# Kernel optimization log

Hardware: AMD Instinct MI355X
Metric: run time of the kernel (lower is better)

The kernel has to match this reference:

```python
import jax, jax.numpy as jnp
import numpy as np

N = 50000
E = 1_600_000
IN_C, HID_C, OUT_C = 128, 64, 16
NEG_SLOPE = 0.2


def setup_inputs() -> dict:
    key = jax.random.key(0)
    ks = jax.random.split(key, 16)
    x = jax.random.normal(ks[0], (N, IN_C), dtype=jnp.float32)
    edge_index = jax.random.randint(ks[1], (2, E), 0, N, dtype=jnp.int32)
    edge_weight = jax.random.uniform(ks[2], (E,), dtype=jnp.float32)

    def lin(k, fan_in, fan_out):
        s = (6.0 / (fan_in + fan_out)) ** 0.5
        return jax.random.uniform(k, (fan_in, fan_out), jnp.float32, -s, s)

    params = {
        "W1": lin(ks[3], IN_C, HID_C),
        "a_src1": jax.random.normal(ks[4], (HID_C,), jnp.float32) * 0.1,
        "a_dst1": jax.random.normal(ks[5], (HID_C,), jnp.float32) * 0.1,
        "b1": jnp.zeros((HID_C,), jnp.float32),
        "W2": lin(ks[6], HID_C, HID_C),
        "a_src2": jax.random.normal(ks[7], (HID_C,), jnp.float32) * 0.1,
        "a_dst2": jax.random.normal(ks[8], (HID_C,), jnp.float32) * 0.1,
        "b2": jnp.zeros((HID_C,), jnp.float32),
        "W3": lin(ks[9], HID_C, OUT_C),
        "a_src3": jax.random.normal(ks[10], (OUT_C,), jnp.float32) * 0.1,
        "a_dst3": jax.random.normal(ks[11], (OUT_C,), jnp.float32) * 0.1,
        "b3": jnp.zeros((OUT_C,), jnp.float32),
    }
    return {"x": x, "edge_index": edge_index, "edge_weight": edge_weight, **params}


def gat_conv(x, W, a_src, a_dst, b, src, dst):
    """Single-head PyG GATConv, add_self_loops=False, eval mode."""
    h = x @ W                                    # [N, C]
    alpha_src = (h * a_src).sum(-1)              # [N]
    alpha_dst = (h * a_dst).sum(-1)              # [N]
    e = jax.nn.leaky_relu(alpha_src[src] + alpha_dst[dst], NEG_SLOPE)  # [E]
    # softmax over incoming edges of each target node
    m = jax.ops.segment_max(e, dst, num_segments=N)
    e = jnp.exp(e - m[dst])
    denom = jax.ops.segment_sum(e, dst, num_segments=N)
    alpha = e / (denom[dst] + 1e-16)             # [E]
    out = jax.ops.segment_sum(h[src] * alpha[:, None], dst, num_segments=N)
    return out + b


def reference(x, edge_index, edge_weight,
              W1, a_src1, a_dst1, b1,
              W2, a_src2, a_dst2, b2,
              W3, a_src3, a_dst3, b3):
    src, dst = edge_index[0], edge_index[1]
    # edge_weight unused: GATConv has no lin_edge (edge_dim=None)
    h = jax.nn.relu(gat_conv(x, W1, a_src1, a_dst1, b1, src, dst))
    h = jax.nn.relu(gat_conv(h, W2, a_src2, a_dst2, b2, src, dst))
    return gat_conv(h, W3, a_src3, a_dst3, b3, src, dst)
```

## Files before the change

### kernel.cpp

```cpp
#include <hip/hip_runtime.h>
#include <hip/hip_fp16.h>
#include <math.h>

#define N_NODES 50000
#define N_EDGES 1600000
#define BSH 8
#define NBUCK ((N_NODES + 255) >> BSH)
#define EPB 4096
#define NBLK ((N_EDGES + EPB - 1) / EPB)


__global__ __launch_bounds__(256) void bucket_hist(const int* __restrict__ dst,
                                                   int* __restrict__ bhist_t, int e) {
    __shared__ int h[NBUCK];
    for (int i = threadIdx.x; i < NBUCK; i += 256) h[i] = 0;
    __syncthreads();
    int base = blockIdx.x * EPB;
#pragma unroll
    for (int j = 0; j < EPB / 256; ++j) {
        int i = base + j * 256 + threadIdx.x;
        if (i < e) atomicAdd(&h[dst[i] >> BSH], 1);
    }
    __syncthreads();
    for (int i = threadIdx.x; i < NBUCK; i += 256)
        bhist_t[i * NBLK + blockIdx.x] = h[i];
}

__global__ __launch_bounds__(256) void bucket_totals(const int* __restrict__ bhist_t,
                                                     int* __restrict__ btot) {
    int b = blockIdx.x;
    const int* col = bhist_t + (size_t)b * NBLK;
    int s = 0;
    for (int i = threadIdx.x; i < NBLK; i += 256) s += col[i];
#pragma unroll
    for (int off = 1; off < 64; off <<= 1) s += __shfl_xor(s, off);
    __shared__ int red[4];
    if ((threadIdx.x & 63) == 0) red[threadIdx.x >> 6] = s;
    __syncthreads();
    if (threadIdx.x == 0)
        btot[b] = red[0] + red[1] + red[2] + red[3];
}

__global__ __launch_bounds__(256) void scan_totals(const int* __restrict__ btot,
                                                   int* __restrict__ bbase,
                                                   int* __restrict__ rowptr) {
    __shared__ int s[256];
    int b = threadIdx.x;
    int v = (b < NBUCK) ? btot[b] : 0;
    s[b] = v;
    __syncthreads();
    for (int off = 1; off < 256; off <<= 1) {
        int t = (b >= off) ? s[b - off] : 0;
        __syncthreads();
        s[b] += t;
        __syncthreads();
    }
    if (b < NBUCK) bbase[b] = s[b] - v;
    if (b == NBUCK - 1) { bbase[NBUCK] = s[b]; rowptr[N_NODES] = s[b]; }
}

__global__ __launch_bounds__(64) void rewrite_offsets(int* __restrict__ bhist_t,
                                                      const int* __restrict__ bbase) {
    int b = blockIdx.x;
    int* col = bhist_t + (size_t)b * NBLK;
    __shared__ int buf[NBLK];
    for (int i = threadIdx.x; i < NBLK; i += 64) buf[i] = col[i];
    __syncthreads();
    constexpr int CH = (NBLK + 63) / 64;
    int lane = threadIdx.x;
    int lo = lane * CH;
    int hi = lo + CH; if (hi > NBLK) hi = NBLK;
    int s = 0;
    for (int i = lo; i < hi; ++i) s += buf[i];
    int inc = s;
#pragma unroll
    for (int off = 1; off < 64; off <<= 1) {
        int t = __shfl_up(inc, off);
        if (lane >= off) inc += t;
    }
    int run = bbase[b] + inc - s;
    for (int i = lo; i < hi; ++i) { int c = buf[i]; col[i] = run; run += c; }
}

__global__ __launch_bounds__(256) void bucket_scatter(const int* __restrict__ src,
                                                      const int* __restrict__ dst,
                                                      const int* __restrict__ bhist_t,
                                                      unsigned* __restrict__ packed, int e) {
    __shared__ int lcur[NBUCK];
    int r = blockIdx.x;
    for (int i = threadIdx.x; i < NBUCK; i += 256)
        lcur[i] = bhist_t[i * NBLK + r];
    __syncthreads();
    int base = r * EPB;
#pragma unroll
    for (int j = 0; j < EPB / 256; ++j) {
        int i = base + j * 256 + threadIdx.x;
        if (i < e) {
            int d = dst[i];
            int pos = atomicAdd(&lcur[d >> BSH], 1);
            packed[pos] = (unsigned)src[i] | ((unsigned)(d & ((1 << BSH) - 1)) << 16);
        }
    }
}

__global__ __launch_bounds__(512) void csr_finalize(const unsigned* __restrict__ packed,
                                                    const int* __restrict__ bbase,
                                                    int* __restrict__ rowptr,
                                                    int* __restrict__ csr_src) {
    int b = blockIdx.x;
    int s0 = bbase[b], s1 = bbase[b + 1];
    int cnt = s1 - s0;
    __shared__ int ncnt[256];
    __shared__ int ncur[256];
    __shared__ int wsum[4];
    if (threadIdx.x < 256) ncnt[threadIdx.x] = 0;
    __syncthreads();
    for (int i = threadIdx.x; i < cnt; i += 512)
        atomicAdd(&ncnt[packed[s0 + i] >> 16], 1);
    __syncthreads();
    int lane = threadIdx.x & 63, w = threadIdx.x >> 6;
    int v = 0, inc = 0;
    if (threadIdx.x < 256) {
        v = ncnt[threadIdx.x]; inc = v;
#pragma unroll
        for (int off = 1; off < 64; off <<= 1) {
            int t = __shfl_up(inc, off);
            if (lane >= off) inc += t;
        }
        if (lane == 63) wsum[w] = inc;
    }
    __syncthreads();
    if (threadIdx.x < 256) {
        int woff = 0;
#pragma unroll
        for (int k = 0; k < 3; ++k) if (k < w) woff += wsum[k];
        int excl = woff + inc - v;
        int node = (b << BSH) + threadIdx.x;
        if (node < N_NODES) rowptr[node] = s0 + excl;
        ncur[threadIdx.x] = s0 + excl;
    }
    __syncthreads();
    for (int i = threadIdx.x; i < cnt; i += 512) {
        unsigned p = packed[s0 + i];
        int pos = atomicAdd(&ncur[p >> 16], 1);
        csr_src[pos] = (int)(p & 0xFFFFu);
    }
}


template<int K, int C, bool HALF_OUT>
__global__ __launch_bounds__(256) void gemm_alpha(
        const float* __restrict__ in, const float* __restrict__ W,
        const float* __restrict__ a_src, const float* __restrict__ a_dst,
        void* __restrict__ hv, float* __restrict__ as_, float* __restrict__ ad_, int n)
{
    constexpr int CPT = C / 16;
    constexpr int KP = K + 4;
    __shared__ float sx[64][KP];
    __shared__ float sW[K * C];
    int row0 = blockIdx.x * 64;
    int nvalid = n - row0;

    for (int idx = threadIdx.x; idx < 64 * K / 4; idx += 256) {
        int r = idx / (K / 4), kc = idx % (K / 4);
        float4 v = {0, 0, 0, 0};
        if (r < nvalid) v = *(const float4*)&in[(size_t)(row0 + r) * K + kc * 4];
        *(float4*)&sx[r][kc * 4] = v;
    }
    for (int idx = threadIdx.x; idx < K * C / 4; idx += 256)
        *(float4*)&sW[idx * 4] = *(const float4*)&W[idx * 4];
    __syncthreads();

    int g  = threadIdx.x >> 4;
    int ci = threadIdx.x & 15;
    int r0 = g * 4;
    int c0 = ci * CPT;

    if constexpr (CPT == 4) {
        float4 acc0 = {0,0,0,0}, acc1 = {0,0,0,0}, acc2 = {0,0,0,0}, acc3 = {0,0,0,0};
        for (int k = 0; k < K; k += 4) {
            float4 w0 = *(const float4*)&sW[(k + 0) * C + c0];
            float4 w1 = *(const float4*)&sW[(k + 1) * C + c0];
            float4 w2 = *(const float4*)&sW[(k + 2) * C + c0];
            float4 w3 = *(const float4*)&sW[(k + 3) * C + c0];
            float4 x0 = *(const float4*)&sx[r0 + 0][k];
            float4 x1 = *(const float4*)&sx[r0 + 1][k];
            float4 x2 = *(const float4*)&sx[r0 + 2][k];
            float4 x3 = *(const float4*)&sx[r0 + 3][k];
#define STEP(A, X) \
            A.x = fmaf(X.x, w0.x, A.x); A.y = fmaf(X.x, w0.y, A.y); \
            A.z = fmaf(X.x, w0.z, A.z); A.w = fmaf(X.x, w0.w, A.w); \
            A.x = fmaf(X.y, w1.x, A.x); A.y = fmaf(X.y, w1.y, A.y); \
            A.z = fmaf(X.y, w1.z, A.z); A.w = fmaf(X.y, w1.w, A.w); \
            A.x = fmaf(X.z, w2.x, A.x); A.y = fmaf(X.z, w2.y, A.y); \
            A.z = fmaf(X.z, w2.z, A.z); A.w = fmaf(X.z, w2.w, A.w); \
            A.x = fmaf(X.w, w3.x, A.x); A.y = fmaf(X.w, w3.y, A.y); \
            A.z = fmaf(X.w, w3.z, A.z); A.w = fmaf(X.w, w3.w, A.w);
            STEP(acc0, x0) STEP(acc1, x1) STEP(acc2, x2) STEP(acc3, x3)
#undef STEP
        }
        if constexpr (HALF_OUT) {
            __half* hh = (__half*)hv;
            auto sth = [&](int r, float4 a) {
                if (r0 + r < nvalid) {
                    size_t base = (size_t)(row0 + r0 + r) * C + c0;
                    *(__half2*)&hh[base]     = __floats2half2_rn(a.x, a.y);
                    *(__half2*)&hh[base + 2] = __floats2half2_rn(a.z, a.w);
                }
            };
            sth(0, acc0); sth(1, acc1); sth(2, acc2); sth(3, acc3);
        } else {
            float* h = (float*)hv;
            if (r0 + 0 < nvalid) *(float4*)&h[(size_t)(row0 + r0 + 0) * C + c0] = acc0;
            if (r0 + 1 < nvalid) *(float4*)&h[(size_t)(row0 + r0 + 1) * C + c0] = acc1;
            if (r0 + 2 < nvalid) *(float4*)&h[(size_t)(row0 + r0 + 2) * C + c0] = acc2;
            if (r0 + 3 < nvalid) *(float4*)&h[(size_t)(row0 + r0 + 3) * C + c0] = acc3;
        }
        float4 asv = *(const float4*)&a_src[c0];
        float4 adv = *(const float4*)&a_dst[c0];
        float vs0 = acc0.x*asv.x + acc0.y*asv.y + acc0.z*asv.z + acc0.w*asv.w;
        float vs1 = acc1.x*asv.x + acc1.y*asv.y + acc1.z*asv.z + acc1.w*asv.w;
        float vs2 = acc2.x*asv.x + acc2.y*asv.y + acc2.z*asv.z + acc2.w*asv.w;
        float vs3 = acc3.x*asv.x + acc3.y*asv.y + acc3.z*asv.z + acc3.w*asv.w;
        float vd0 = acc0.x*adv.x + acc0.y*adv.y + acc0.z*adv.z + acc0.w*adv.w;
        float vd1 = acc1.x*adv.x + acc1.y*adv.y + acc1.z*adv.z + acc1.w*adv.w;
        float vd2 = acc2.x*adv.x + acc2.y*adv.y + acc2.z*adv.z + acc2.w*adv.w;
        float vd3 = acc3.x*adv.x + acc3.y*adv.y + acc3.z*adv.z + acc3.w*adv.w;
#pragma unroll
        for (int off = 1; off < 16; off <<= 1) {
            vs0 += __shfl_xor(vs0, off); vs1 += __shfl_xor(vs1, off);
            vs2 += __shfl_xor(vs2, off); vs3 += __shfl_xor(vs3, off);
            vd0 += __shfl_xor(vd0, off); vd1 += __shfl_xor(vd1, off);
            vd2 += __shfl_xor(vd2, off); vd3 += __shfl_xor(vd3, off);
        }
        if (ci == 0) {
            if (r0 + 0 < nvalid) { as_[row0+r0+0] = vs0; ad_[row0+r0+0] = vd0; }
            if (r0 + 1 < nvalid) { as_[row0+r0+1] = vs1; ad_[row0+r0+1] = vd1; }
            if (r0 + 2 < nvalid) { as_[row0+r0+2] = vs2; ad_[row0+r0+2] = vd2; }
            if (r0 + 3 < nvalid) { as_[row0+r0+3] = vs3; ad_[row0+r0+3] = vd3; }
        }
    } else {
        float* h = (float*)hv;
        float s0 = 0.f, s1 = 0.f, s2 = 0.f, s3 = 0.f;
        for (int k = 0; k < K; k += 4) {
            float w0 = sW[(k + 0) * C + c0];
            float w1 = sW[(k + 1) * C + c0];
            float w2 = sW[(k + 2) * C + c0];
            float w3 = sW[(k + 3) * C + c0];
            float4 x0 = *(const float4*)&sx[r0 + 0][k];
            float4 x1 = *(const float4*)&sx[r0 + 1][k];
            float4 x2 = *(const float4*)&sx[r0 + 2][k];
            float4 x3 = *(const float4*)&sx[r0 + 3][k];
            s0 = fmaf(x0.x,w0, fmaf(x0.y,w1, fmaf(x0.z,w2, fmaf(x0.w,w3, s0))));
            s1 = fmaf(x1.x,w0, fmaf(x1.y,w1, fmaf(x1.z,w2, fmaf(x1.w,w3, s1))));
            s2 = fmaf(x2.x,w0, fmaf(x2.y,w1, fmaf(x2.z,w2, fmaf(x2.w,w3, s2))));
            s3 = fmaf(x3.x,w0, fmaf(x3.y,w1, fmaf(x3.z,w2, fmaf(x3.w,w3, s3))));
        }
        if (r0 + 0 < nvalid) h[(size_t)(row0+r0+0) * C + c0] = s0;
        if (r0 + 1 < nvalid) h[(size_t)(row0+r0+1) * C + c0] = s1;
        if (r0 + 2 < nvalid) h[(size_t)(row0+r0+2) * C + c0] = s2;
        if (r0 + 3 < nvalid) h[(size_t)(row0+r0+3) * C + c0] = s3;
        float as0 = a_src[c0], ad0 = a_dst[c0];
        float vs0 = s0*as0, vs1 = s1*as0, vs2 = s2*as0, vs3 = s3*as0;
        float vd0 = s0*ad0, vd1 = s1*ad0, vd2 = s2*ad0, vd3 = s3*ad0;
#pragma unroll
        for (int off = 1; off < 16; off <<= 1) {
            vs0 += __shfl_xor(vs0, off); vs1 += __shfl_xor(vs1, off);
            vs2 += __shfl_xor(vs2, off); vs3 += __shfl_xor(vs3, off);
            vd0 += __shfl_xor(vd0, off); vd1 += __shfl_xor(vd1, off);
            vd2 += __shfl_xor(vd2, off); vd3 += __shfl_xor(vd3, off);
        }
        if (ci == 0) {
            if (r0 + 0 < nvalid) { as_[row0+r0+0] = vs0; ad_[row0+r0+0] = vd0; }
            if (r0 + 1 < nvalid) { as_[row0+r0+1] = vs1; ad_[row0+r0+1] = vd1; }
            if (r0 + 2 < nvalid) { as_[row0+r0+2] = vs2; ad_[row0+r0+2] = vd2; }
            if (r0 + 3 < nvalid) { as_[row0+r0+3] = vs3; ad_[row0+r0+3] = vd3; }
        }
    }
}


__device__ __forceinline__ float leaky(float e) {
    return (e >= 0.f) ? e : 0.2f * e;
}

template<bool RELU>
__global__ __launch_bounds__(256) void agg64h(
        const __half* __restrict__ h, const float* __restrict__ as_, const float* __restrict__ ad_,
        const int* __restrict__ rowptr, const int* __restrict__ csr_src,
        const float* __restrict__ bias, float* __restrict__ out, int n)
{
    int node = (blockIdx.x * blockDim.x + threadIdx.x) >> 6;
    if (node >= n) return;
    int lane = threadIdx.x & 63;
    int g  = lane >> 3;
    int c8 = lane & 7;
    int start = rowptr[node], end = rowptr[node + 1];
    float adn = ad_[node];
    const char* hb = (const char*)h + (size_t)c8 * 16;

    float4 accL = {0,0,0,0}, accH = {0,0,0,0};
    float dsum = 0.f;

#define HACC(R, W) { \
    float2 f0 = __half22float2(*(__half2*)&R.x); \
    float2 f1 = __half22float2(*(__half2*)&R.y); \
    float2 f2 = __half22float2(*(__half2*)&R.z); \
    float2 f3 = __half22float2(*(__half2*)&R.w); \
    accL.x = fmaf(W, f0.x, accL.x); accL.y = fmaf(W, f0.y, accL.y); \
    accL.z = fmaf(W, f1.x, accL.z); accL.w = fmaf(W, f1.y, accL.w); \
    accH.x = fmaf(W, f2.x, accH.x); accH.y = fmaf(W, f2.y, accH.y); \
    accH.z = fmaf(W, f3.x, accH.z); accH.w = fmaf(W, f3.y, accH.w); }

    for (int chunk = start; chunk < end; chunk += 64) {
        int e_i = chunk + lane;
        int soff = 0; float aw = 0.f;
        if (e_i < end) {
            int ssrc = csr_src[e_i];
            soff = ssrc << 7;
            aw = __expf(leaky(as_[ssrc] + adn));
        }
        dsum += aw;
        int nv = end - chunk; if (nv > 64) nv = 64;
        int nvu = (nv + 31) & ~31;
        for (int j = g; j < nvu; j += 32) {
            int   o0 = __shfl(soff, j),      o1 = __shfl(soff, j + 8);
            int   o2 = __shfl(soff, j + 16), o3 = __shfl(soff, j + 24);
            float w0 = __shfl(aw, j),        w1 = __shfl(aw, j + 8);
            float w2 = __shfl(aw, j + 16),   w3 = __shfl(aw, j + 24);
            uint4 r0 = *(const uint4*)(hb + o0);
            uint4 r1 = *(const uint4*)(hb + o1);
            uint4 r2 = *(const uint4*)(hb + o2);
            uint4 r3 = *(const uint4*)(hb + o3);
            HACC(r0, w0) HACC(r1, w1) HACC(r2, w2) HACC(r3, w3)
        }
    }
#undef HACC
#pragma unroll
    for (int off = 8; off <= 32; off <<= 1) {
        accL.x += __shfl_xor(accL.x, off); accL.y += __shfl_xor(accL.y, off);
        accL.z += __shfl_xor(accL.z, off); accL.w += __shfl_xor(accL.w, off);
        accH.x += __shfl_xor(accH.x, off); accH.y += __shfl_xor(accH.y, off);
        accH.z += __shfl_xor(accH.z, off); accH.w += __shfl_xor(accH.w, off);
    }
#pragma unroll
    for (int off = 1; off <= 32; off <<= 1) dsum += __shfl_xor(dsum, off);

    if (g == 0) {
        float inv = 1.f / (dsum + 1e-16f);
        float4 bl = *(const float4*)&bias[c8 * 8];
        float4 bh = *(const float4*)&bias[c8 * 8 + 4];
        float4 ol, oh;
        ol.x = fmaf(accL.x, inv, bl.x); ol.y = fmaf(accL.y, inv, bl.y);
        ol.z = fmaf(accL.z, inv, bl.z); ol.w = fmaf(accL.w, inv, bl.w);
        oh.x = fmaf(accH.x, inv, bh.x); oh.y = fmaf(accH.y, inv, bh.y);
        oh.z = fmaf(accH.z, inv, bh.z); oh.w = fmaf(accH.w, inv, bh.w);
        if (RELU) {
            ol.x = fmaxf(ol.x, 0.f); ol.y = fmaxf(ol.y, 0.f);
            ol.z = fmaxf(ol.z, 0.f); ol.w = fmaxf(ol.w, 0.f);
            oh.x = fmaxf(oh.x, 0.f); oh.y = fmaxf(oh.y, 0.f);
            oh.z = fmaxf(oh.z, 0.f); oh.w = fmaxf(oh.w, 0.f);
        }
        *(float4*)&out[(size_t)node * 64 + c8 * 8]     = ol;
        *(float4*)&out[(size_t)node * 64 + c8 * 8 + 4] = oh;
    }
}

template<bool RELU>
__global__ __launch_bounds__(256) void agg16(
        const float* __restrict__ h, const float* __restrict__ as_, const float* __restrict__ ad_,
        const int* __restrict__ rowptr, const int* __restrict__ csr_src,
        const float* __restrict__ bias, float* __restrict__ out, int n)
{
    int node = (blockIdx.x * blockDim.x + threadIdx.x) >> 6;
    if (node >= n) return;
    int lane = threadIdx.x & 63;
    int g  = lane >> 2;
    int c4 = lane & 3;
    int start = rowptr[node], end = rowptr[node + 1];
    float adn = ad_[node];
    const char* hb = (const char*)h + (size_t)c4 * 16;

    float4 acc = {0,0,0,0};
    float dsum = 0.f;

    for (int chunk = start; chunk < end; chunk += 64) {
        int e_i = chunk + lane;
        int soff = 0; float aw = 0.f;
        if (e_i < end) {
            int ssrc = csr_src[e_i];
            soff = ssrc << 6;
            aw = __expf(leaky(as_[ssrc] + adn));
        }
        dsum += aw;
        int nv = end - chunk; if (nv > 64) nv = 64;
        int nvu = (nv + 31) & ~31;
        for (int j = g; j < nvu; j += 32) {
            int   o0 = __shfl(soff, j);
            int   o1 = __shfl(soff, j + 16);
            float w0 = __shfl(aw, j);
            float w1 = __shfl(aw, j + 16);
            float4 h0 = *(const float4*)(hb + o0);
            float4 h1 = *(const float4*)(hb + o1);
            acc.x = fmaf(w0, h0.x, acc.x); acc.y = fmaf(w0, h0.y, acc.y);
            acc.z = fmaf(w0, h0.z, acc.z); acc.w = fmaf(w0, h0.w, acc.w);
            acc.x = fmaf(w1, h1.x, acc.x); acc.y = fmaf(w1, h1.y, acc.y);
            acc.z = fmaf(w1, h1.z, acc.z); acc.w = fmaf(w1, h1.w, acc.w);
        }
    }
#pragma unroll
    for (int off = 4; off <= 32; off <<= 1) {
        acc.x += __shfl_xor(acc.x, off); acc.y += __shfl_xor(acc.y, off);
        acc.z += __shfl_xor(acc.z, off); acc.w += __shfl_xor(acc.w, off);
    }
#pragma unroll
    for (int off = 1; off <= 32; off <<= 1) dsum += __shfl_xor(dsum, off);

    if (g == 0) {
        float inv = 1.f / (dsum + 1e-16f);
        float4 bv = *(const float4*)&bias[c4 * 4];
        float4 o;
        o.x = fmaf(acc.x, inv, bv.x); o.y = fmaf(acc.y, inv, bv.y);
        o.z = fmaf(acc.z, inv, bv.z); o.w = fmaf(acc.w, inv, bv.w);
        if (RELU) {
            o.x = fmaxf(o.x, 0.f); o.y = fmaxf(o.y, 0.f);
            o.z = fmaxf(o.z, 0.f); o.w = fmaxf(o.w, 0.f);
        }
        *(float4*)&out[(size_t)node * 16 + c4 * 4] = o;
    }
}


extern "C" void kernel_launch(void* const* d_in, const int* in_sizes, int n_in,
                              void* d_out, int out_size, void* d_ws, size_t ws_size,
                              hipStream_t stream) {
    const float* x   = (const float*)d_in[0];
    const int*   ei  = (const int*)  d_in[1];
    const float* W1  = (const float*)d_in[3];
    const float* as1 = (const float*)d_in[4];
    const float* ad1 = (const float*)d_in[5];
    const float* b1  = (const float*)d_in[6];
    const float* W2  = (const float*)d_in[7];
    const float* as2 = (const float*)d_in[8];
    const float* ad2 = (const float*)d_in[9];
    const float* b2  = (const float*)d_in[10];
    const float* W3  = (const float*)d_in[11];
    const float* as3 = (const float*)d_in[12];
    const float* ad3 = (const float*)d_in[13];
    const float* b3  = (const float*)d_in[14];

    const int* srcp = ei;
    const int* dstp = ei + N_EDGES;

    char* ws = (char*)d_ws;
    size_t off = 0;
    auto alloc = [&](size_t bytes) -> void* {
        void* p = ws + off;
        off = (off + bytes + 255) & ~(size_t)255;
        return p;
    };
    int*   bhist_t = (int*)  alloc((size_t)NBUCK * NBLK * sizeof(int));
    int*   btot    = (int*)  alloc(NBUCK * sizeof(int));
    int*   bbase   = (int*)  alloc((NBUCK + 1) * sizeof(int));
    int*   rowptr  = (int*)  alloc((N_NODES + 1) * sizeof(int));
    int*   csr_src = (int*)  alloc(N_EDGES * sizeof(int));
    float* asb     = (float*)alloc(N_NODES * sizeof(float));
    float* adb     = (float*)alloc(N_NODES * sizeof(float));
    __half* hHalf  = (__half*)alloc((size_t)N_NODES * 64 * sizeof(__half));
    float* bufA    = (float*)alloc((size_t)N_NODES * 64 * sizeof(float));
    float* bufB    = (float*)alloc((size_t)N_NODES * 64 * sizeof(float));
    unsigned* packed = (unsigned*)bufA;

    bucket_hist    <<<NBLK,  256, 0, stream>>>(dstp, bhist_t, N_EDGES);
    bucket_totals  <<<NBUCK, 256, 0, stream>>>(bhist_t, btot);
    scan_totals    <<<1,     256, 0, stream>>>(btot, bbase, rowptr);
    rewrite_offsets<<<NBUCK, 64,  0, stream>>>(bhist_t, bbase);
    bucket_scatter <<<NBLK,  256, 0, stream>>>(srcp, dstp, bhist_t, packed, N_EDGES);
    csr_finalize   <<<NBUCK, 512, 0, stream>>>(packed, bbase, rowptr, csr_src);

    const int NB64 = (N_NODES + 63) / 64;
    const int NB4  = (N_NODES + 3) / 4;

    gemm_alpha<128, 64, true><<<NB64, 256, 0, stream>>>(x, W1, as1, ad1, hHalf, asb, adb, N_NODES);
    agg64h<true><<<NB4, 256, 0, stream>>>(hHalf, asb, adb, rowptr, csr_src, b1, bufA, N_NODES);

    gemm_alpha<64, 64, true><<<NB64, 256, 0, stream>>>(bufA, W2, as2, ad2, hHalf, asb, adb, N_NODES);
    agg64h<true><<<NB4, 256, 0, stream>>>(hHalf, asb, adb, rowptr, csr_src, b2, bufA, N_NODES);

    gemm_alpha<64, 16, false><<<NB64, 256, 0, stream>>>(bufA, W3, as3, ad3, bufB, asb, adb, N_NODES);
    agg16<false><<<NB4, 256, 0, stream>>>(bufB, asb, adb, rowptr, csr_src, b3, (float*)d_out, N_NODES);
}
```

Measured before the change: 185.3 us.

## Store intermediate activations and layer-3 features in fp16, fold bucket scan into consumers

The outputs of the first two aggregation layers are now written as fp16 and read as fp16 by the following GEMM, and the layer-3 projected features are stored in fp16 so the final aggregation gathers half-width rows. The single-block scan kernel is removed: each rewrite_offsets and csr_finalize block recomputes its bucket prefix directly from the bucket totals. The packed edge buffer gets its own allocation. This cuts gather and activation memory traffic and one launch, at the cost of extra fp16 rounding error and redundant prefix sums per block.

```diff
diff --git a/kernel.cpp b/kernel.cpp
--- a/kernel.cpp
+++ b/kernel.cpp
@@ -41,33 +41,22 @@
         btot[b] = red[0] + red[1] + red[2] + red[3];
 }
 
-__global__ __launch_bounds__(256) void scan_totals(const int* __restrict__ btot,
-                                                   int* __restrict__ bbase,
-                                                   int* __restrict__ rowptr) {
-    __shared__ int s[256];
-    int b = threadIdx.x;
-    int v = (b < NBUCK) ? btot[b] : 0;
-    s[b] = v;
-    __syncthreads();
-    for (int off = 1; off < 256; off <<= 1) {
-        int t = (b >= off) ? s[b - off] : 0;
-        __syncthreads();
-        s[b] += t;
-        __syncthreads();
-    }
-    if (b < NBUCK) bbase[b] = s[b] - v;
-    if (b == NBUCK - 1) { bbase[NBUCK] = s[b]; rowptr[N_NODES] = s[b]; }
-}
-
 __global__ __launch_bounds__(64) void rewrite_offsets(int* __restrict__ bhist_t,
-                                                      const int* __restrict__ bbase) {
+                                                      const int* __restrict__ btot,
+                                                      int* __restrict__ rowptr) {
     int b = blockIdx.x;
+    int lane = threadIdx.x;
+    int pre = 0;
+    for (int i = lane; i < NBUCK; i += 64) if (i < b) pre += btot[i];
+#pragma unroll
+    for (int off = 1; off < 64; off <<= 1) pre += __shfl_xor(pre, off);
+    if (b == 0 && lane == 0) rowptr[N_NODES] = N_EDGES;
+
     int* col = bhist_t + (size_t)b * NBLK;
     __shared__ int buf[NBLK];
-    for (int i = threadIdx.x; i < NBLK; i += 64) buf[i] = col[i];
+    for (int i = lane; i < NBLK; i += 64) buf[i] = col[i];
     __syncthreads();
     constexpr int CH = (NBLK + 63) / 64;
-    int lane = threadIdx.x;
     int lo = lane * CH;
     int hi = lo + CH; if (hi > NBLK) hi = NBLK;
     int s = 0;
@@ -78,7 +67,7 @@
         int t = __shfl_up(inc, off);
         if (lane >= off) inc += t;
     }
-    int run = bbase[b] + inc - s;
+    int run = pre + inc - s;
     for (int i = lo; i < hi; ++i) { int c = buf[i]; col[i] = run; run += c; }
 }
 
@@ -104,11 +93,27 @@
 }
 
 __global__ __launch_bounds__(512) void csr_finalize(const unsigned* __restrict__ packed,
-                                                    const int* __restrict__ bbase,
+                                                    const int* __restrict__ btot,
                                                     int* __restrict__ rowptr,
                                                     int* __restrict__ csr_src) {
     int b = blockIdx.x;
-    int s0 = bbase[b], s1 = bbase[b + 1];
+    __shared__ int sb[2];
+    if (threadIdx.x < 64) {
+        int pre = 0, tot = 0;
+        for (int i = threadIdx.x; i < NBUCK; i += 64) {
+            int v = btot[i];
+            if (i < b) pre += v;
+            if (i == b) tot = v;
+        }
+#pragma unroll
+        for (int off = 1; off < 64; off <<= 1) {
+            pre += __shfl_xor(pre, off);
+            tot += __shfl_xor(tot, off);
+        }
+        if (threadIdx.x == 0) { sb[0] = pre; sb[1] = pre + tot; }
+    }
+    __syncthreads();
+    int s0 = sb[0], s1 = sb[1];
     int cnt = s1 - s0;
     __shared__ int ncnt[256];
     __shared__ int ncur[256];
@@ -148,9 +153,9 @@
 }
 
 
-template<int K, int C, bool HALF_OUT>
+template<int K, int C, bool IN_HALF, bool OUT_HALF>
 __global__ __launch_bounds__(256) void gemm_alpha(
-        const float* __restrict__ in, const float* __restrict__ W,
+        const void* __restrict__ inv, const float* __restrict__ W,
         const float* __restrict__ a_src, const float* __restrict__ a_dst,
         void* __restrict__ hv, float* __restrict__ as_, float* __restrict__ ad_, int n)
 {
@@ -161,11 +166,28 @@
     int row0 = blockIdx.x * 64;
     int nvalid = n - row0;
 
-    for (int idx = threadIdx.x; idx < 64 * K / 4; idx += 256) {
-        int r = idx / (K / 4), kc = idx % (K / 4);
-        float4 v = {0, 0, 0, 0};
-        if (r < nvalid) v = *(const float4*)&in[(size_t)(row0 + r) * K + kc * 4];
-        *(float4*)&sx[r][kc * 4] = v;
+    if constexpr (IN_HALF) {
+        const __half* inh = (const __half*)inv;
+        for (int idx = threadIdx.x; idx < 64 * K / 8; idx += 256) {
+            int r = idx / (K / 8), kc = idx % (K / 8);
+            uint4 v = {0u, 0u, 0u, 0u};
+            if (r < nvalid) v = *(const uint4*)&inh[(size_t)(row0 + r) * K + kc * 8];
+            float2 f0 = __half22float2(*(__half2*)&v.x);
+            float2 f1 = __half22float2(*(__half2*)&v.y);
+            float2 f2 = __half22float2(*(__half2*)&v.z);
+            float2 f3 = __half22float2(*(__half2*)&v.w);
+            float* d = &sx[r][kc * 8];
+            d[0] = f0.x; d[1] = f0.y; d[2] = f1.x; d[3] = f1.y;
+            d[4] = f2.x; d[5] = f2.y; d[6] = f3.x; d[7] = f3.y;
+        }
+    } else {
+        const float* in = (const float*)inv;
+        for (int idx = threadIdx.x; idx < 64 * K / 4; idx += 256) {
+            int r = idx / (K / 4), kc = idx % (K / 4);
+            float4 v = {0, 0, 0, 0};
+            if (r < nvalid) v = *(const float4*)&in[(size_t)(row0 + r) * K + kc * 4];
+            *(float4*)&sx[r][kc * 4] = v;
+        }
     }
     for (int idx = threadIdx.x; idx < K * C / 4; idx += 256)
         *(float4*)&sW[idx * 4] = *(const float4*)&W[idx * 4];
@@ -199,7 +221,7 @@
             STEP(acc0, x0) STEP(acc1, x1) STEP(acc2, x2) STEP(acc3, x3)
 #undef STEP
         }
-        if constexpr (HALF_OUT) {
+        if constexpr (OUT_HALF) {
             __half* hh = (__half*)hv;
             auto sth = [&](int r, float4 a) {
                 if (r0 + r < nvalid) {
@@ -240,7 +262,6 @@
             if (r0 + 3 < nvalid) { as_[row0+r0+3] = vs3; ad_[row0+r0+3] = vd3; }
         }
     } else {
-        float* h = (float*)hv;
         float s0 = 0.f, s1 = 0.f, s2 = 0.f, s3 = 0.f;
         for (int k = 0; k < K; k += 4) {
             float w0 = sW[(k + 0) * C + c0];
@@ -256,10 +277,19 @@
             s2 = fmaf(x2.x,w0, fmaf(x2.y,w1, fmaf(x2.z,w2, fmaf(x2.w,w3, s2))));
             s3 = fmaf(x3.x,w0, fmaf(x3.y,w1, fmaf(x3.z,w2, fmaf(x3.w,w3, s3))));
         }
-        if (r0 + 0 < nvalid) h[(size_t)(row0+r0+0) * C + c0] = s0;
-        if (r0 + 1 < nvalid) h[(size_t)(row0+r0+1) * C + c0] = s1;
-        if (r0 + 2 < nvalid) h[(size_t)(row0+r0+2) * C + c0] = s2;
-        if (r0 + 3 < nvalid) h[(size_t)(row0+r0+3) * C + c0] = s3;
+        if constexpr (OUT_HALF) {
+            __half* hh = (__half*)hv;
+            if (r0 + 0 < nvalid) hh[(size_t)(row0+r0+0) * C + c0] = __float2half_rn(s0);
+            if (r0 + 1 < nvalid) hh[(size_t)(row0+r0+1) * C + c0] = __float2half_rn(s1);
+            if (r0 + 2 < nvalid) hh[(size_t)(row0+r0+2) * C + c0] = __float2half_rn(s2);
+            if (r0 + 3 < nvalid) hh[(size_t)(row0+r0+3) * C + c0] = __float2half_rn(s3);
+        } else {
+            float* h = (float*)hv;
+            if (r0 + 0 < nvalid) h[(size_t)(row0+r0+0) * C + c0] = s0;
+            if (r0 + 1 < nvalid) h[(size_t)(row0+r0+1) * C + c0] = s1;
+            if (r0 + 2 < nvalid) h[(size_t)(row0+r0+2) * C + c0] = s2;
+            if (r0 + 3 < nvalid) h[(size_t)(row0+r0+3) * C + c0] = s3;
+        }
         float as0 = a_src[c0], ad0 = a_dst[c0];
         float vs0 = s0*as0, vs1 = s1*as0, vs2 = s2*as0, vs3 = s3*as0;
         float vd0 = s0*ad0, vd1 = s1*ad0, vd2 = s2*ad0, vd3 = s3*ad0;
@@ -284,11 +314,22 @@
     return (e >= 0.f) ? e : 0.2f * e;
 }
 
+__device__ __forceinline__ void hacc8(uint4 r, float w, float4& accL, float4& accH) {
+    float2 f0 = __half22float2(*(__half2*)&r.x);
+    float2 f1 = __half22float2(*(__half2*)&r.y);
+    float2 f2 = __half22float2(*(__half2*)&r.z);
+    float2 f3 = __half22float2(*(__half2*)&r.w);
+    accL.x = fmaf(w, f0.x, accL.x); accL.y = fmaf(w, f0.y, accL.y);
+    accL.z = fmaf(w, f1.x, accL.z); accL.w = fmaf(w, f1.y, accL.w);
+    accH.x = fmaf(w, f2.x, accH.x); accH.y = fmaf(w, f2.y, accH.y);
+    accH.z = fmaf(w, f3.x, accH.z); accH.w = fmaf(w, f3.y, accH.w);
+}
+
 template<bool RELU>
 __global__ __launch_bounds__(256) void agg64h(
         const __half* __restrict__ h, const float* __restrict__ as_, const float* __restrict__ ad_,
         const int* __restrict__ rowptr, const int* __restrict__ csr_src,
-        const float* __restrict__ bias, float* __restrict__ out, int n)
+        const float* __restrict__ bias, __half* __restrict__ out, int n)
 {
     int node = (blockIdx.x * blockDim.x + threadIdx.x) >> 6;
     if (node >= n) return;
@@ -301,16 +342,6 @@
 
     float4 accL = {0,0,0,0}, accH = {0,0,0,0};
     float dsum = 0.f;
-
-#define HACC(R, W) { \
-    float2 f0 = __half22float2(*(__half2*)&R.x); \
-    float2 f1 = __half22float2(*(__half2*)&R.y); \
-    float2 f2 = __half22float2(*(__half2*)&R.z); \
-    float2 f3 = __half22float2(*(__half2*)&R.w); \
-    accL.x = fmaf(W, f0.x, accL.x); accL.y = fmaf(W, f0.y, accL.y); \
-    accL.z = fmaf(W, f1.x, accL.z); accL.w = fmaf(W, f1.y, accL.w); \
-    accH.x = fmaf(W, f2.x, accH.x); accH.y = fmaf(W, f2.y, accH.y); \
-    accH.z = fmaf(W, f3.x, accH.z); accH.w = fmaf(W, f3.y, accH.w); }
 
     for (int chunk = start; chunk < end; chunk += 64) {
         int e_i = chunk + lane;
@@ -332,10 +363,10 @@
             uint4 r1 = *(const uint4*)(hb + o1);
             uint4 r2 = *(const uint4*)(hb + o2);
             uint4 r3 = *(const uint4*)(hb + o3);
-            HACC(r0, w0) HACC(r1, w1) HACC(r2, w2) HACC(r3, w3)
-        }
-    }
-#undef HACC
+            hacc8(r0, w0, accL, accH); hacc8(r1, w1, accL, accH);
+            hacc8(r2, w2, accL, accH); hacc8(r3, w3, accL, accH);
+        }
+    }
 #pragma unroll
     for (int off = 8; off <= 32; off <<= 1) {
         accL.x += __shfl_xor(accL.x, off); accL.y += __shfl_xor(accL.y, off);
@@ -361,27 +392,33 @@
             oh.x = fmaxf(oh.x, 0.f); oh.y = fmaxf(oh.y, 0.f);
             oh.z = fmaxf(oh.z, 0.f); oh.w = fmaxf(oh.w, 0.f);
         }
-        *(float4*)&out[(size_t)node * 64 + c8 * 8]     = ol;
-        *(float4*)&out[(size_t)node * 64 + c8 * 8 + 4] = oh;
+        __half2 p0 = __floats2half2_rn(ol.x, ol.y);
+        __half2 p1 = __floats2half2_rn(ol.z, ol.w);
+        __half2 p2 = __floats2half2_rn(oh.x, oh.y);
+        __half2 p3 = __floats2half2_rn(oh.z, oh.w);
+        uint4 pk;
+        pk.x = *(unsigned*)&p0; pk.y = *(unsigned*)&p1;
+        pk.z = *(unsigned*)&p2; pk.w = *(unsigned*)&p3;
+        *(uint4*)&out[(size_t)node * 64 + c8 * 8] = pk;
     }
 }
 
 template<bool RELU>
-__global__ __launch_bounds__(256) void agg16(
-        const float* __restrict__ h, const float* __restrict__ as_, const float* __restrict__ ad_,
+__global__ __launch_bounds__(256) void agg16h(
+        const __half* __restrict__ h, const float* __restrict__ as_, const float* __restrict__ ad_,
         const int* __restrict__ rowptr, const int* __restrict__ csr_src,
         const float* __restrict__ bias, float* __restrict__ out, int n)
 {
     int node = (blockIdx.x * blockDim.x + threadIdx.x) >> 6;
     if (node >= n) return;
     int lane = threadIdx.x & 63;
-    int g  = lane >> 2;
-    int c4 = lane & 3;
+    int g   = lane >> 1;
+    int c16 = lane & 1;
     int start = rowptr[node], end = rowptr[node + 1];
     float adn = ad_[node];
-    const char* hb = (const char*)h + (size_t)c4 * 16;
-
-    float4 acc = {0,0,0,0};
+    const char* hb = (const char*)h + (size_t)c16 * 16;
+
+    float4 accL = {0,0,0,0}, accH = {0,0,0,0};
     float dsum = 0.f;
 
     for (int chunk = start; chunk < end; chunk += 64) {
@@ -389,7 +426,7 @@
         int soff = 0; float aw = 0.f;
         if (e_i < end) {
             int ssrc = csr_src[e_i];
-            soff = ssrc << 6;
+            soff = ssrc << 5;
             aw = __expf(leaky(as_[ssrc] + adn));
         }
         dsum += aw;
@@ -397,36 +434,38 @@
         int nvu = (nv + 31) & ~31;
         for (int j = g; j < nvu; j += 32) {
             int   o0 = __shfl(soff, j);
-            int   o1 = __shfl(soff, j + 16);
             float w0 = __shfl(aw, j);
-            float w1 = __shfl(aw, j + 16);
-            float4 h0 = *(const float4*)(hb + o0);
-            float4 h1 = *(const float4*)(hb + o1);
-            acc.x = fmaf(w0, h0.x, acc.x); acc.y = fmaf(w0, h0.y, acc.y);
-            acc.z = fmaf(w0, h0.z, acc.z); acc.w = fmaf(w0, h0.w, acc.w);
-            acc.x = fmaf(w1, h1.x, acc.x); acc.y = fmaf(w1, h1.y, acc.y);
-            acc.z = fmaf(w1, h1.z, acc.z); acc.w = fmaf(w1, h1.w, acc.w);
-        }
-    }
-#pragma unroll
-    for (int off = 4; off <= 32; off <<= 1) {
-        acc.x += __shfl_xor(acc.x, off); acc.y += __shfl_xor(acc.y, off);
-        acc.z += __shfl_xor(acc.z, off); acc.w += __shfl_xor(acc.w, off);
+            uint4 r0 = *(const uint4*)(hb + o0);
+            hacc8(r0, w0, accL, accH);
+        }
+    }
+#pragma unroll
+    for (int off = 2; off <= 32; off <<= 1) {
+        accL.x += __shfl_xor(accL.x, off); accL.y += __shfl_xor(accL.y, off);
+        accL.z += __shfl_xor(accL.z, off); accL.w += __shfl_xor(accL.w, off);
+        accH.x += __shfl_xor(accH.x, off); accH.y += __shfl_xor(accH.y, off);
+        accH.z += __shfl_xor(accH.z, off); accH.w += __shfl_xor(accH.w, off);
     }
 #pragma unroll
     for (int off = 1; off <= 32; off <<= 1) dsum += __shfl_xor(dsum, off);
 
     if (g == 0) {
         float inv = 1.f / (dsum + 1e-16f);
-        float4 bv = *(const float4*)&bias[c4 * 4];
-        float4 o;
-        o.x = fmaf(acc.x, inv, bv.x); o.y = fmaf(acc.y, inv, bv.y);
-        o.z = fmaf(acc.z, inv, bv.z); o.w = fmaf(acc.w, inv, bv.w);
+        float4 bl = *(const float4*)&bias[c16 * 8];
+        float4 bh = *(const float4*)&bias[c16 * 8 + 4];
+        float4 ol, oh;
+        ol.x = fmaf(accL.x, inv, bl.x); ol.y = fmaf(accL.y, inv, bl.y);
+        ol.z = fmaf(accL.z, inv, bl.z); ol.w = fmaf(accL.w, inv, bl.w);
+        oh.x = fmaf(accH.x, inv, bh.x); oh.y = fmaf(accH.y, inv, bh.y);
+        oh.z = fmaf(accH.z, inv, bh.z); oh.w = fmaf(accH.w, inv, bh.w);
         if (RELU) {
-            o.x = fmaxf(o.x, 0.f); o.y = fmaxf(o.y, 0.f);
-            o.z = fmaxf(o.z, 0.f); o.w = fmaxf(o.w, 0.f);
-        }
-        *(float4*)&out[(size_t)node * 16 + c4 * 4] = o;
+            ol.x = fmaxf(ol.x, 0.f); ol.y = fmaxf(ol.y, 0.f);
+            ol.z = fmaxf(ol.z, 0.f); ol.w = fmaxf(ol.w, 0.f);
+            oh.x = fmaxf(oh.x, 0.f); oh.y = fmaxf(oh.y, 0.f);
+            oh.z = fmaxf(oh.z, 0.f); oh.w = fmaxf(oh.w, 0.f);
+        }
+        *(float4*)&out[(size_t)node * 16 + c16 * 8]     = ol;
+        *(float4*)&out[(size_t)node * 16 + c16 * 8 + 4] = oh;
     }
 }
 
@@ -459,34 +498,32 @@
         off = (off + bytes + 255) & ~(size_t)255;
         return p;
     };
-    int*   bhist_t = (int*)  alloc((size_t)NBUCK * NBLK * sizeof(int));
-    int*   btot    = (int*)  alloc(NBUCK * sizeof(int));
-    int*   bbase   = (int*)  alloc((NBUCK + 1) * sizeof(int));
-    int*   rowptr  = (int*)  alloc((N_NODES + 1) * sizeof(int));
-    int*   csr_src = (int*)  alloc(N_EDGES * sizeof(int));
-    float* asb     = (float*)alloc(N_NODES * sizeof(float));
-    float* adb     = (float*)alloc(N_NODES * sizeof(float));
+    int*   bhist_t = (int*)   alloc((size_t)NBUCK * NBLK * sizeof(int));
+    int*   btot    = (int*)   alloc(NBUCK * sizeof(int));
+    int*   rowptr  = (int*)   alloc((N_NODES + 1) * sizeof(int));
+    int*   csr_src = (int*)   alloc(N_EDGES * sizeof(int));
+    float* asb     = (float*) alloc(N_NODES * sizeof(float));
+    float* adb     = (float*) alloc(N_NODES * sizeof(float));
     __half* hHalf  = (__half*)alloc((size_t)N_NODES * 64 * sizeof(__half));
-    float* bufA    = (float*)alloc((size_t)N_NODES * 64 * sizeof(float));
-    float* bufB    = (float*)alloc((size_t)N_NODES * 64 * sizeof(float));
-    unsigned* packed = (unsigned*)bufA;
+    __half* aHalf  = (__half*)alloc((size_t)N_NODES * 64 * sizeof(__half));
+    __half* h16    = (__half*)alloc((size_t)N_NODES * 16 * sizeof(__half));
+    unsigned* packed = (unsigned*)alloc((size_t)N_EDGES * sizeof(unsigned));
 
     bucket_hist    <<<NBLK,  256, 0, stream>>>(dstp, bhist_t, N_EDGES);
     bucket_totals  <<<NBUCK, 256, 0, stream>>>(bhist_t, btot);
-    scan_totals    <<<1,     256, 0, stream>>>(btot, bbase, rowptr);
-    rewrite_offsets<<<NBUCK, 64,  0, stream>>>(bhist_t, bbase);
+    rewrite_offsets<<<NBUCK, 64,  0, stream>>>(bhist_t, btot, rowptr);
     bucket_scatter <<<NBLK,  256, 0, stream>>>(srcp, dstp, bhist_t, packed, N_EDGES);
-    csr_finalize   <<<NBUCK, 512, 0, stream>>>(packed, bbase, rowptr, csr_src);
+    csr_finalize   <<<NBUCK, 512, 0, stream>>>(packed, btot, rowptr, csr_src);
 
     const int NB64 = (N_NODES + 63) / 64;
     const int NB4  = (N_NODES + 3) / 4;
 
-    gemm_alpha<128, 64, true><<<NB64, 256, 0, stream>>>(x, W1, as1, ad1, hHalf, asb, adb, N_NODES);
-    agg64h<true><<<NB4, 256, 0, stream>>>(hHalf, asb, adb, rowptr, csr_src, b1, bufA, N_NODES);
-
-    gemm_alpha<64, 64, true><<<NB64, 256, 0, stream>>>(bufA, W2, as2, ad2, hHalf, asb, adb, N_NODES);
-    agg64h<true><<<NB4, 256, 0, stream>>>(hHalf, asb, adb, rowptr, csr_src, b2, bufA, N_NODES);
-
-    gemm_alpha<64, 16, false><<<NB64, 256, 0, stream>>>(bufA, W3, as3, ad3, bufB, asb, adb, N_NODES);
-    agg16<false><<<NB4, 256, 0, stream>>>(bufB, asb, adb, rowptr, csr_src, b3, (float*)d_out, N_NODES);
-}
+    gemm_alpha<128, 64, false, true><<<NB64, 256, 0, stream>>>(x, W1, as1, ad1, hHalf, asb, adb, N_NODES);
+    agg64h<true><<<NB4, 256, 0, stream>>>(hHalf, asb, adb, rowptr, csr_src, b1, aHalf, N_NODES);
+
+    gemm_alpha<64, 64, true, true><<<NB64, 256, 0, stream>>>(aHalf, W2, as2, ad2, hHalf, asb, adb, N_NODES);
+    agg64h<true><<<NB4, 256, 0, stream>>>(hHalf, asb, adb, rowptr, csr_src, b2, aHalf, N_NODES);
+
+    gemm_alpha<64, 16, true, true><<<NB64, 256, 0, stream>>>(aHalf, W3, as3, ad3, h16, asb, adb, N_NODES);
+    agg16h<false><<<NB4, 256, 0, stream>>>(h16, asb, adb, rowptr, csr_src, b3, (float*)d_out, N_NODES);
+}
```

Result: slower. 189.5 us (+2.3%).
